# Optimization experiments

Hardware: AMD Instinct MI355X
Metric: run time of the kernel (lower is better)

The kernel has to match this reference:

```python
import jax, jax.numpy as jnp
import numpy as np

D_MODEL = 1024
N_HEADS = 16
D_HEAD = D_MODEL // N_HEADS
D_FF = 4096
BATCH = 2
SEQ = 2048
LN_EPS = 1e-5


def setup_inputs() -> dict:
    key = jax.random.key(0)
    ks = jax.random.split(key, 12)
    s = 1.0 / np.sqrt(D_MODEL)
    x = jax.random.normal(ks[0], (BATCH, SEQ, D_MODEL), dtype=jnp.float32)
    mask = jnp.broadcast_to(jnp.tril(jnp.ones((SEQ, SEQ), jnp.int32)), (BATCH, SEQ, SEQ))
    return {
        "x": x,
        "mask": mask,
        # per-head projections stacked: [H, D, Dh] (bias=False in source)
        "Wq": jax.random.normal(ks[1], (N_HEADS, D_MODEL, D_HEAD), jnp.float32) * s,
        "Wk": jax.random.normal(ks[2], (N_HEADS, D_MODEL, D_HEAD), jnp.float32) * s,
        "Wv": jax.random.normal(ks[3], (N_HEADS, D_MODEL, D_HEAD), jnp.float32) * s,
        "Wo": jax.random.normal(ks[4], (D_MODEL, D_MODEL), jnp.float32) * s,
        "ln1_w": jnp.ones((D_MODEL,), jnp.float32),
        "ln1_b": jnp.zeros((D_MODEL,), jnp.float32),
        "ln2_w": jnp.ones((D_MODEL,), jnp.float32),
        "ln2_b": jnp.zeros((D_MODEL,), jnp.float32),
        "W1": jax.random.normal(ks[5], (D_MODEL, D_FF), jnp.float32) * s,
        "b1": jnp.zeros((D_FF,), jnp.float32),
        "W2": jax.random.normal(ks[6], (D_FF, D_MODEL), jnp.float32) * (1.0 / np.sqrt(D_FF)),
        "b2": jnp.zeros((D_MODEL,), jnp.float32),
    }


def layer_norm(x, w, b):
    mu = jnp.mean(x, axis=-1, keepdims=True)
    var = jnp.var(x, axis=-1, keepdims=True)
    return (x - mu) * jax.lax.rsqrt(var + LN_EPS) * w + b


def reference(x, mask, Wq, Wk, Wv, Wo, ln1_w, ln1_b, ln2_w, ln2_b, W1, b1, W2, b2):
    # pre-LN masked self-attention
    h = layer_norm(x, ln1_w, ln1_b)
    q = jnp.einsum("bsd,hde->bhse", h, Wq)  # [B,H,S,Dh]
    k = jnp.einsum("bsd,hde->bhse", h, Wk)
    v = jnp.einsum("bsd,hde->bhse", h, Wv)
    scores = jnp.einsum("bhse,bhte->bhst", q, k) / np.sqrt(D_HEAD)
    scores = jnp.where(mask[:, None, :, :].astype(bool), scores, -jnp.inf)
    weights = jax.nn.softmax(scores, axis=-1)
    attn = jnp.einsum("bhst,bhte->bhse", weights, v)  # [B,H,S,Dh]
    # concat heads (head order = last-dim order in torch.cat)
    concat = attn.transpose(0, 2, 1, 3).reshape(x.shape[0], x.shape[1], D_MODEL)
    att_out = concat @ Wo
    att_x = x + att_out
    # FFN with exact (erf) GELU, matching nn.GELU default
    h2 = layer_norm(att_x, ln2_w, ln2_b)
    ff = jax.nn.gelu(h2 @ W1 + b1, approximate=False) @ W2 + b2
    return att_x + ff
```

## Files before the change

### kernel.cpp

```cpp
#include <hip/hip_runtime.h>
#include <hip/hip_bf16.h>
#include <math.h>

#define D_MODEL 1024
#define N_HEADS 16
#define D_HEAD  64
#define D_FF    4096
#define BATCH   2
#define SEQ     2048
#define NTOK    (BATCH*SEQ)

typedef __hip_bfloat16 bf16;
typedef __attribute__((ext_vector_type(8))) short short8;
typedef __attribute__((ext_vector_type(4))) float floatx4;

template<typename TIN>
__global__ void ln_kernel(const TIN* __restrict__ x,
                          const float* __restrict__ w,
                          const float* __restrict__ b,
                          bf16* __restrict__ out) {
    int row = blockIdx.x;
    int tid = threadIdx.x;
    const long base = (long)row * D_MODEL;
    float v[4];
    float s = 0.f, sq = 0.f;
#pragma unroll
    for (int i = 0; i < 4; ++i) {
        float xv = (float)x[base + tid + i*256];
        v[i] = xv; s += xv; sq += xv*xv;
    }
    __shared__ float r1[256], r2[256];
    r1[tid] = s; r2[tid] = sq; __syncthreads();
    for (int off = 128; off > 0; off >>= 1) {
        if (tid < off) { r1[tid] += r1[tid+off]; r2[tid] += r2[tid+off]; }
        __syncthreads();
    }
    float mean = r1[0] * (1.f/D_MODEL);
    float var  = r2[0] * (1.f/D_MODEL) - mean*mean;
    float rstd = rsqrtf(var + 1e-5f);
#pragma unroll
    for (int i = 0; i < 4; ++i) {
        int c = tid + i*256;
        out[base + c] = __float2bfloat16((v[i] - mean) * rstd * w[c] + b[c]);
    }
}

__global__ __launch_bounds__(256) void wcvt_kernel(const float* __restrict__ W,
                                                   bf16* __restrict__ Wt,
                                                   int K, int N) {
    __shared__ float t[32][33];
    int n0 = blockIdx.x * 32, k0 = blockIdx.y * 32;
    int lx = threadIdx.x & 31, ly = threadIdx.x >> 5;
#pragma unroll
    for (int i = 0; i < 4; ++i) {
        int k = ly + i * 8;
        t[k][lx] = W[(long)(k0 + k) * N + n0 + lx];
    }
    __syncthreads();
#pragma unroll
    for (int i = 0; i < 4; ++i) {
        int n = ly + i * 8;
        Wt[(long)(n0 + n) * K + k0 + lx] = __float2bfloat16(t[lx][n]);
    }
}

__global__ __launch_bounds__(256) void wcvt_wo_w1(const float* __restrict__ Wo,
                                                  const float* __restrict__ W1,
                                                  bf16* __restrict__ wo_bf,
                                                  bf16* __restrict__ w1_bf) {
    __shared__ float t[32][33];
    int gx = blockIdx.x;
    const float* W; bf16* Wt; int N, n0;
    if (gx < 32) { W = Wo; Wt = wo_bf; N = D_MODEL; n0 = gx * 32; }
    else         { W = W1; Wt = w1_bf; N = D_FF;    n0 = (gx - 32) * 32; }
    int k0 = blockIdx.y * 32;
    int lx = threadIdx.x & 31, ly = threadIdx.x >> 5;
#pragma unroll
    for (int i = 0; i < 4; ++i) {
        int k = ly + i * 8;
        t[k][lx] = W[(long)(k0 + k) * N + n0 + lx];
    }
    __syncthreads();
#pragma unroll
    for (int i = 0; i < 4; ++i) {
        int n = ly + i * 8;
        Wt[(long)(n0 + n) * D_MODEL + k0 + lx] = __float2bfloat16(t[lx][n]);
    }
}

__global__ __launch_bounds__(256) void wcvt_qkv(const float* __restrict__ Wq,
                                                const float* __restrict__ Wk,
                                                const float* __restrict__ Wv,
                                                bf16* __restrict__ outp) {
    __shared__ float t[32][33];
    int z = blockIdx.z, mat = z >> 4, head = z & 15;
    const float* W = (mat == 0 ? Wq : mat == 1 ? Wk : Wv) + (long)head * D_MODEL * D_HEAD;
    bf16* Wt = outp + (long)z * D_HEAD * D_MODEL;
    int n0 = blockIdx.x * 32, k0 = blockIdx.y * 32;
    int lx = threadIdx.x & 31, ly = threadIdx.x >> 5;
#pragma unroll
    for (int i = 0; i < 4; ++i) {
        int k = ly + i * 8;
        t[k][lx] = W[(long)(k0 + k) * D_HEAD + n0 + lx];
    }
    __syncthreads();
#pragma unroll
    for (int i = 0; i < 4; ++i) {
        int n = ly + i * 8;
        Wt[(long)(n0 + n) * D_MODEL + k0 + lx] = __float2bfloat16(t[lx][n]);
    }
}

__device__ inline void swz2d(int& bx, int& by) {
    int gx = gridDim.x;
    int nwg = gx * gridDim.y;
    int bid = blockIdx.y * gx + blockIdx.x;
    int swz = (bid & 7) * (nwg >> 3) + (bid >> 3);
    bx = swz % gx;
    by = swz / gx;
}

template<int ROWS>
__device__ inline void stage_tile(const bf16* g, int gstride, short* lds) {
    int lane = threadIdx.x & 63, wave = threadIdx.x >> 6;
#pragma unroll
    for (int it = 0; it < ROWS / 64; ++it) {
        int c = wave + it * 4;
        const bf16* gp = g + (long)(c * 16 + (lane >> 2)) * gstride + (lane & 3) * 8;
        short* lp = lds + c * 512 + lane * 8;
        __builtin_amdgcn_global_load_lds(
            (const __attribute__((address_space(1))) void*)gp,
            (__attribute__((address_space(3))) void*)lp, 16, 0, 0);
    }
}

template<int BM, int BN, int BK>
__device__ inline void gemm_accum(const bf16* __restrict__ A, int lda,
                                  const bf16* __restrict__ Wt, int K,
                                  int row0, int col0, short* As, short* Bs,
                                  floatx4 (&acc)[BM/32][BN/32]) {
    constexpr int MI  = BM / 32;
    constexpr int NR  = BN / 32;
    constexpr int ASZ = BM * BK;
    constexpr int BSZ = BN * BK;
    int tid  = threadIdx.x;
    int wave = tid >> 6, lane = tid & 63;
    int quad = lane >> 4, l16 = lane & 15;
    int wm = (wave >> 1) * (BM / 2);
    int wn = (wave & 1) * (BN / 2);

    auto stage = [&](int k0, int buf) {
#pragma unroll
        for (int kk = 0; kk < BK; kk += 32) {
            stage_tile<BM>(A  + (long)row0 * lda + k0 + kk, lda,
                           As + buf * ASZ + (kk / 32) * BM * 32);
            stage_tile<BN>(Wt + (long)col0 * K   + k0 + kk, K,
                           Bs + buf * BSZ + (kk / 32) * BN * 32);
        }
    };

    stage(0, 0);
    __syncthreads();

    int cur = 0;
    for (int k0 = 0; k0 < K; k0 += BK) {
        if (k0 + BK < K) stage(k0 + BK, cur ^ 1);

#pragma unroll
        for (int p = 0; p < BK / 32; ++p) {
            const short* Ap = As + cur * ASZ + p * BM * 32;
            const short* Bp = Bs + cur * BSZ + p * BN * 32;
            short8 af[MI], bfr[NR];
#pragma unroll
            for (int mi = 0; mi < MI; ++mi)
                af[mi] = *(const short8*)&Ap[(wm + mi * 16 + l16) * 32 + quad * 8];
#pragma unroll
            for (int ni = 0; ni < NR; ++ni)
                bfr[ni] = *(const short8*)&Bp[(wn + ni * 16 + l16) * 32 + quad * 8];
#pragma unroll
            for (int mi = 0; mi < MI; ++mi)
#pragma unroll
                for (int ni = 0; ni < NR; ++ni)
                    acc[mi][ni] = __builtin_amdgcn_mfma_f32_16x16x32_bf16(
                        af[mi], bfr[ni], acc[mi][ni], 0, 0, 0);
        }
        __syncthreads();
        cur ^= 1;
    }
}

template<int BM, int BN, int BK, int BIAS, int ACT, int RES, int OUTBF16>
__global__ __launch_bounds__(256) void mfma_gemm_bf(
    const bf16* __restrict__ A, int lda,
    const bf16* __restrict__ Wt, int K,
    const float* __restrict__ bias, const float* __restrict__ resid,
    void* __restrict__ Cout, int ldc)
{
    constexpr int MI = BM / 32;
    constexpr int NR = BN / 32;
    __shared__ short As[2 * BM * BK];
    __shared__ short Bs[2 * BN * BK];
    int bx, by; swz2d(bx, by);
    int row0 = by * BM, col0 = bx * BN;
    int tid = threadIdx.x, wave = tid >> 6, lane = tid & 63;
    int quad = lane >> 4, l16 = lane & 15;
    int wm = (wave >> 1) * (BM / 2);
    int wn = (wave & 1) * (BN / 2);

    floatx4 acc[MI][NR];
#pragma unroll
    for (int mi = 0; mi < MI; ++mi)
#pragma unroll
        for (int ni = 0; ni < NR; ++ni)
            acc[mi][ni] = (floatx4){0.f, 0.f, 0.f, 0.f};

    gemm_accum<BM, BN, BK>(A, lda, Wt, K, row0, col0, As, Bs, acc);

#pragma unroll
    for (int mi = 0; mi < MI; ++mi) {
#pragma unroll
        for (int ni = 0; ni < NR; ++ni) {
#pragma unroll
            for (int r = 0; r < 4; ++r) {
                int row = row0 + wm + mi * 16 + quad * 4 + r;
                int col = col0 + wn + ni * 16 + l16;
                float v = acc[mi][ni][r];
                if (BIAS) v += bias[col];
                if (ACT == 1) {
                    float x2 = v * v;
                    float arg = fminf(v * fmaf(0.1029392f, x2, 2.3021182f), 20.f);
                    float t = exp2f(arg);
                    v = v * t * __builtin_amdgcn_rcpf(t + 1.f);
                }
                long idx = (long)row * ldc + col;
                if (RES == 1) v += resid[idx];
                if (OUTBF16) ((bf16*)Cout)[idx] = __float2bfloat16(v);
                else         ((float*)Cout)[idx] = v;
            }
        }
    }
}


struct QkvOut { bf16* o[3]; };

#define RG(buf,mat,kh) (((buf)*4 + (mat)*2 + (kh)) * 8192)
#define G256_BAR  asm volatile("s_barrier" ::: "memory")
#define G256_VM4  asm volatile("s_waitcnt vmcnt(4)" ::: "memory")
#define G256_VM0  asm volatile("s_waitcnt vmcnt(0)" ::: "memory")

__device__ inline void stage2(const bf16* g0, const bf16* g1, int koff, short* lp) {
    __builtin_amdgcn_global_load_lds(
        (const __attribute__((address_space(1))) void*)(g0 + koff),
        (__attribute__((address_space(3))) void*)lp, 16, 0, 0);
    __builtin_amdgcn_global_load_lds(
        (const __attribute__((address_space(1))) void*)(g1 + koff),
        (__attribute__((address_space(3))) void*)(lp + 4096), 16, 0, 0);
}

template<int MH>
__device__ inline void rd_frags(const short* lds, int ra, int rb,
                                int wr, int wc, int l16, int quad,
                                short8 (&areg)[4], short8 (&breg)[4]) {
    if (MH == 0) {
#pragma unroll
        for (int ni = 0; ni < 4; ++ni) {
            int row = wc * 64 + ni * 16 + l16;
            int sl = quad ^ ((row >> 1) & 3);
            breg[ni] = *(const short8*)&lds[rb + row * 32 + sl * 8];
        }
    }
#pragma unroll
    for (int mi = 0; mi < 4; ++mi) {
        int row = wr * 128 + (MH * 4 + mi) * 16 + l16;
        int sl = quad ^ ((row >> 1) & 3);
        areg[mi] = *(const short8*)&lds[ra + row * 32 + sl * 8];
    }
}

template<int MH>
__device__ inline void do_mfma16(const short8 (&areg)[4], const short8 (&breg)[4],
                                 floatx4 (&acc)[8][4]) {
    __builtin_amdgcn_s_setprio(1);
#pragma unroll
    for (int mi = 0; mi < 4; ++mi)
#pragma unroll
        for (int ni = 0; ni < 4; ++ni)
            acc[MH * 4 + mi][ni] = __builtin_amdgcn_mfma_f32_16x16x32_bf16(
                areg[mi], breg[ni], acc[MH * 4 + mi][ni], 0, 0, 0);
    __builtin_amdgcn_s_setprio(0);
}

template<int EPI>
__global__ __launch_bounds__(512, 1) void gemm256_kernel(
    const bf16* __restrict__ A, int lda,
    const bf16* __restrict__ Wt, int K,
    const float* __restrict__ bias,
    bf16* __restrict__ Cout, int ldc, QkvOut qa)
{
    __shared__ short lds[65536];
    const int NT = K / 64;
    int row0 = blockIdx.y * 256, col0 = blockIdx.x * 256;
    int tid = threadIdx.x;
    int lane = tid & 63, wave = tid >> 6;
    int quad = lane >> 4, l16 = lane & 15;
    int wr = wave >> 2, wc = wave & 3;

    int srow = tid >> 2, slot = tid & 3;
    int cA0 = slot ^ ((srow >> 1) & 3);
    int cA1 = slot ^ (((srow + 128) >> 1) & 3);
    const bf16* a0 = A  + (long)(row0 + srow) * lda + cA0 * 8;
    const bf16* a1 = A  + (long)(row0 + srow + 128) * lda + cA1 * 8;
    const bf16* b0 = Wt + (long)(col0 + srow) * K + cA0 * 8;
    const bf16* b1 = Wt + (long)(col0 + srow + 128) * K + cA1 * 8;
    short* lt = lds + tid * 8;

    floatx4 acc[8][4];
#pragma unroll
    for (int mi = 0; mi < 8; ++mi)
#pragma unroll
        for (int ni = 0; ni < 4; ++ni)
            acc[mi][ni] = (floatx4){0.f, 0.f, 0.f, 0.f};

    stage2(a0, a1, 0,  lt + RG(0,0,0));
    stage2(b0, b1, 0,  lt + RG(0,1,0));
    stage2(a0, a1, 32, lt + RG(0,0,1));
    stage2(b0, b1, 32, lt + RG(0,1,1));
    stage2(a0, a1, 64, lt + RG(1,0,0));
    stage2(b0, b1, 64, lt + RG(1,1,0));
    G256_VM4;
    G256_BAR;

    short8 areg[4], breg[4];

    for (int i = 0; i < NT / 2; ++i) {
        int T = 2 * i;
        bool s2 = (T + 2 < NT);
        bool s3 = (T + 3 < NT);
        int k1off = (T + 1) * 64;
        int k2off = (T + 2) * 64;
        int k3off = (T + 3) * 64;

        rd_frags<0>(lds, RG(0,0,0), RG(0,1,0), wr, wc, l16, quad, areg, breg);
        stage2(a0, a1, k1off + 32, lt + RG(1,0,1));
        G256_BAR;
        do_mfma16<0>(areg, breg, acc);
        G256_BAR;

        rd_frags<1>(lds, RG(0,0,0), RG(0,1,0), wr, wc, l16, quad, areg, breg);
        stage2(b0, b1, k1off + 32, lt + RG(1,1,1));
        G256_BAR;
        do_mfma16<1>(areg, breg, acc);
        G256_BAR;

        rd_frags<0>(lds, RG(0,0,1), RG(0,1,1), wr, wc, l16, quad, areg, breg);
        if (s2) stage2(a0, a1, k2off, lt + RG(0,0,0));
        G256_BAR;
        do_mfma16<0>(areg, breg, acc);
        G256_BAR;

        rd_frags<1>(lds, RG(0,0,1), RG(0,1,1), wr, wc, l16, quad, areg, breg);
        if (s2) stage2(b0, b1, k2off, lt + RG(0,1,0));
        G256_BAR;
        do_mfma16<1>(areg, breg, acc);
        if (s2) { G256_VM4; } else { G256_VM0; }
        G256_BAR;

        rd_frags<0>(lds, RG(1,0,0), RG(1,1,0), wr, wc, l16, quad, areg, breg);
        if (s2) stage2(a0, a1, k2off + 32, lt + RG(0,0,1));
        G256_BAR;
        do_mfma16<0>(areg, breg, acc);
        G256_BAR;

        rd_frags<1>(lds, RG(1,0,0), RG(1,1,0), wr, wc, l16, quad, areg, breg);
        if (s2) stage2(b0, b1, k2off + 32, lt + RG(0,1,1));
        G256_BAR;
        do_mfma16<1>(areg, breg, acc);
        G256_BAR;

        rd_frags<0>(lds, RG(1,0,1), RG(1,1,1), wr, wc, l16, quad, areg, breg);
        if (s3) stage2(a0, a1, k3off, lt + RG(1,0,0));
        G256_BAR;
        do_mfma16<0>(areg, breg, acc);
        G256_BAR;

        rd_frags<1>(lds, RG(1,0,1), RG(1,1,1), wr, wc, l16, quad, areg, breg);
        if (s3) stage2(b0, b1, k3off, lt + RG(1,1,0));
        G256_BAR;
        do_mfma16<1>(areg, breg, acc);
        if (s3) { G256_VM4; } else { G256_VM0; }
        G256_BAR;
    }

#pragma unroll
    for (int mi = 0; mi < 8; ++mi) {
#pragma unroll
        for (int ni = 0; ni < 4; ++ni) {
#pragma unroll
            for (int r = 0; r < 4; ++r) {
                int row = row0 + wr * 128 + mi * 16 + quad * 4 + r;
                int col = col0 + wc * 64 + ni * 16 + l16;
                float v = acc[mi][ni][r];
                if constexpr (EPI == 0) {
                    v += bias[col];
                    float x2 = v * v;
                    float arg = fminf(v * fmaf(0.1029392f, x2, 2.3021182f), 20.f);
                    float t = exp2f(arg);
                    v = v * t * __builtin_amdgcn_rcpf(t + 1.f);
                    Cout[(long)row * ldc + col] = __float2bfloat16(v);
                } else {
                    int mat = col >> 10, hd = (col >> 6) & 15, d = col & 63;
                    int b = row >> 11, s = row & 2047;
                    qa.o[mat][(((long)(b * 16 + hd) * SEQ + s) << 6) + d] =
                        __float2bfloat16(v);
                }
            }
        }
    }
}

__global__ __launch_bounds__(256) void fattn_mfma(const bf16* __restrict__ q,
                                                  const bf16* __restrict__ k,
                                                  const bf16* __restrict__ v,
                                                  bf16* __restrict__ po,
                                                  float* __restrict__ lz) {
    int byr = blockIdx.y;
    int tile = (byr < 8) ? byr : 23 - byr;
    int chunk = blockIdx.z;
    int bh = blockIdx.x;
    int tid = threadIdx.x;
    int wave = tid >> 6, lane = tid & 63;
    int quad = lane >> 4, l16 = lane & 15;
    const long base = (long)bh * SEQ * D_HEAD;
    const int r0g = tile * 128;

    bf16*  pob = po + (long)chunk * 32 * SEQ * 64;
    float* lzb = lz + (long)chunk * 32 * SEQ;

    __shared__ short Ks[64 * 72];
    __shared__ short Vt[64 * 72];
    __shared__ short Ps[4][32 * 72];

    short8 qf[2][2];
#pragma unroll
    for (int rb = 0; rb < 2; ++rb) {
        const short* qrow = (const short*)(q + base +
            (long)(r0g + wave * 32 + rb * 16 + l16) * D_HEAD);
        qf[rb][0] = *(const short8*)(qrow + quad * 8);
        qf[rb][1] = *(const short8*)(qrow + 32 + quad * 8);
#pragma unroll
        for (int c = 0; c < 2; ++c)
#pragma unroll
            for (int j = 0; j < 8; ++j) {
                float f = __uint_as_float(((unsigned)(unsigned short)qf[rb][c][j]) << 16)
                          * 0.18033688f;
                qf[rb][c][j] = __builtin_bit_cast(short, __float2bfloat16(f));
            }
    }

    short8 onesf;
    {
        short o1 = (l16 == 0) ? (short)0x3F80 : (short)0;
#pragma unroll
        for (int j = 0; j < 8; ++j) onesf[j] = o1;
    }

    floatx4 o[2][4];
#pragma unroll
    for (int rb = 0; rb < 2; ++rb)
#pragma unroll
        for (int nb = 0; nb < 4; ++nb) o[rb][nb] = (floatx4){0.f, 0.f, 0.f, 0.f};
    floatx4 l4[2] = {(floatx4){0.f,0.f,0.f,0.f}, (floatx4){0.f,0.f,0.f,0.f}};

    const int kt0 = chunk ? tile + 1 : 0;
    const int kt1 = chunk ? 2 * tile + 1 : tile;
    for (int kt = kt0; kt <= kt1; ++kt) {
        __syncthreads();
        {
            int t = tid >> 2, c = tid & 3;
            const short* krow = (const short*)(k + base + (long)(kt * 64 + t) * D_HEAD);
            *(uint4*)&Ks[t * 72 + c * 16]     = *(const uint4*)(krow + c * 16);
            *(uint4*)&Ks[t * 72 + c * 16 + 8] = *(const uint4*)(krow + c * 16 + 8);
        }
        {
            int tp = (tid & 31) * 2;
            int d0 = ((tid >> 5) & 7) * 8;
            const short* v0 = (const short*)(v + base + (long)(kt * 64 + tp) * D_HEAD + d0);
            short va[8], vb[8];
            *(uint4*)va = *(const uint4*)v0;
            *(uint4*)vb = *(const uint4*)(v0 + D_HEAD);
#pragma unroll
            for (int j = 0; j < 8; ++j) {
                unsigned pk = (unsigned)(unsigned short)va[j] |
                              ((unsigned)(unsigned short)vb[j] << 16);
                *(unsigned*)&Vt[(d0 + j) * 72 + tp] = pk;
            }
        }
        __syncthreads();

        if (kt * 64 > r0g + wave * 32 + 31) continue;

        floatx4 s[2][4];
#pragma unroll
        for (int nb = 0; nb < 4; ++nb) {
            short8 kf0 = *(const short8*)&Ks[(nb * 16 + l16) * 72 + quad * 8];
            short8 kf1 = *(const short8*)&Ks[(nb * 16 + l16) * 72 + 32 + quad * 8];
#pragma unroll
            for (int rb = 0; rb < 2; ++rb) {
                floatx4 z4 = (floatx4){0.f, 0.f, 0.f, 0.f};
                z4 = __builtin_amdgcn_mfma_f32_16x16x32_bf16(qf[rb][0], kf0, z4, 0, 0, 0);
                z4 = __builtin_amdgcn_mfma_f32_16x16x32_bf16(qf[rb][1], kf1, z4, 0, 0, 0);
                s[rb][nb] = z4;
            }
        }

        if (kt >= 2 * tile) {
#pragma unroll
            for (int rb = 0; rb < 2; ++rb) {
                int qg = r0g + wave * 32 + rb * 16 + quad * 4;
#pragma unroll
                for (int nb = 0; nb < 4; ++nb) {
                    int kg = kt * 64 + nb * 16 + l16;
#pragma unroll
                    for (int r = 0; r < 4; ++r)
                        if (kg > qg + r) s[rb][nb][r] = -1e30f;
                }
            }
        }

        short* Pw = &Ps[wave][0];
#pragma unroll
        for (int rb = 0; rb < 2; ++rb)
#pragma unroll
            for (int nb = 0; nb < 4; ++nb)
#pragma unroll
                for (int r = 0; r < 4; ++r) {
                    float p = exp2f(s[rb][nb][r]);
                    Pw[(rb * 16 + quad * 4 + r) * 72 + nb * 16 + l16] =
                        __builtin_bit_cast(short, __float2bfloat16(p));
                }

        short8 pf[2][2];
#pragma unroll
        for (int rb = 0; rb < 2; ++rb) {
            pf[rb][0] = *(const short8*)&Pw[(rb * 16 + l16) * 72 + quad * 8];
            pf[rb][1] = *(const short8*)&Pw[(rb * 16 + l16) * 72 + 32 + quad * 8];
        }
#pragma unroll
        for (int nb = 0; nb < 4; ++nb) {
            short8 vf0 = *(const short8*)&Vt[(nb * 16 + l16) * 72 + quad * 8];
            short8 vf1 = *(const short8*)&Vt[(nb * 16 + l16) * 72 + 32 + quad * 8];
#pragma unroll
            for (int rb = 0; rb < 2; ++rb) {
                o[rb][nb] = __builtin_amdgcn_mfma_f32_16x16x32_bf16(pf[rb][0], vf0, o[rb][nb], 0, 0, 0);
                o[rb][nb] = __builtin_amdgcn_mfma_f32_16x16x32_bf16(pf[rb][1], vf1, o[rb][nb], 0, 0, 0);
            }
        }
#pragma unroll
        for (int rb = 0; rb < 2; ++rb) {
            l4[rb] = __builtin_amdgcn_mfma_f32_16x16x32_bf16(pf[rb][0], onesf, l4[rb], 0, 0, 0);
            l4[rb] = __builtin_amdgcn_mfma_f32_16x16x32_bf16(pf[rb][1], onesf, l4[rb], 0, 0, 0);
        }
    }

#pragma unroll
    for (int rb = 0; rb < 2; ++rb) {
#pragma unroll
        for (int nb = 0; nb < 4; ++nb)
#pragma unroll
            for (int r = 0; r < 4; ++r) {
                int row = r0g + wave * 32 + rb * 16 + quad * 4 + r;
                pob[((long)bh * SEQ + row) * 64 + nb * 16 + l16] =
                    __float2bfloat16(o[rb][nb][r]);
            }
        if (l16 == 0) {
#pragma unroll
            for (int r = 0; r < 4; ++r) {
                int row = r0g + wave * 32 + rb * 16 + quad * 4 + r;
                lzb[(long)bh * SEQ + row] = l4[rb][r];
            }
        }
    }
}

__global__ __launch_bounds__(256) void attn_combine(const bf16* __restrict__ po,
                                                    const float* __restrict__ lz,
                                                    bf16* __restrict__ cc) {
    const long CH = 32L * SEQ * 64;
    int row = blockIdx.x;
    int b = row >> 11, s = row & 2047;
    int tid = threadIdx.x;
    int col = tid * 4;
    int h = col >> 6, d = col & 63;
    long pidx = ((long)(b * 16 + h) * SEQ + s) * 64 + d;
    uint2 u0 = *(const uint2*)((const unsigned short*)po + pidx);
    uint2 u1 = *(const uint2*)((const unsigned short*)po + CH + pidx);
    long li = (long)(b * 16 + h) * SEQ + s;
    float linv = 1.f / (lz[li] + lz[32L * SEQ + li]);
    unsigned ua[4] = {u0.x & 0xFFFFu, u0.x >> 16, u0.y & 0xFFFFu, u0.y >> 16};
    unsigned ub[4] = {u1.x & 0xFFFFu, u1.x >> 16, u1.y & 0xFFFFu, u1.y >> 16};
    unsigned short rr[4];
#pragma unroll
    for (int i = 0; i < 4; ++i) {
        float ov = __uint_as_float(ua[i] << 16) + __uint_as_float(ub[i] << 16);
        rr[i] = __builtin_bit_cast(unsigned short, __float2bfloat16(ov * linv));
    }
    uint2 w;
    w.x = (unsigned)rr[0] | ((unsigned)rr[1] << 16);
    w.y = (unsigned)rr[2] | ((unsigned)rr[3] << 16);
    *(uint2*)((unsigned short*)cc + (long)row * D_MODEL + col) = w;
}

extern "C" void kernel_launch(void* const* d_in, const int* in_sizes, int n_in,
                              void* d_out, int out_size, void* d_ws, size_t ws_size,
                              hipStream_t stream) {
    const float* x    = (const float*)d_in[0];
    const float* Wq   = (const float*)d_in[2];
    const float* Wk   = (const float*)d_in[3];
    const float* Wv   = (const float*)d_in[4];
    const float* Wo   = (const float*)d_in[5];
    const float* ln1w = (const float*)d_in[6];
    const float* ln1b = (const float*)d_in[7];
    const float* ln2w = (const float*)d_in[8];
    const float* ln2b = (const float*)d_in[9];
    const float* W1   = (const float*)d_in[10];
    const float* b1   = (const float*)d_in[11];
    const float* W2   = (const float*)d_in[12];
    const float* b2   = (const float*)d_in[13];
    float* out = (float*)d_out;

    char* wsb = (char*)d_ws;
    const size_t MB = 1024*1024;
    bf16*  h1      = (bf16*)(wsb + 0*MB);
    bf16*  qb      = (bf16*)(wsb + 8*MB);
    bf16*  kb      = (bf16*)(wsb + 16*MB);
    bf16*  vb      = (bf16*)(wsb + 24*MB);
    bf16*  wqkv_bf = (bf16*)(wsb + 32*MB);
    bf16*  po      = (bf16*)(wsb + 32*MB);
    float* lz      = (float*)(wsb + 48*MB);
    bf16*  cc      = (bf16*)(wsb + 0*MB);
    bf16*  wo_bf   = (bf16*)(wsb + 8*MB);
    bf16*  w1_bf   = (bf16*)(wsb + 10*MB);
    bf16*  h2      = (bf16*)(wsb + 0*MB);
    bf16*  ff      = (bf16*)(wsb + 24*MB);
    bf16*  w2_bf   = (bf16*)(wsb + 8*MB);

    QkvOut qa; qa.o[0] = qb; qa.o[1] = kb; qa.o[2] = vb;
    QkvOut qdummy = {};

    ln_kernel<float><<<NTOK, 256, 0, stream>>>(x, ln1w, ln1b, h1);

    wcvt_qkv<<<dim3(2, 32, 48), 256, 0, stream>>>(Wq, Wk, Wv, wqkv_bf);

    gemm256_kernel<1><<<dim3(12, 16), 512, 0, stream>>>(
        h1, D_MODEL, wqkv_bf, D_MODEL, nullptr, nullptr, 0, qa);

    fattn_mfma<<<dim3(BATCH*N_HEADS, SEQ/128, 2), 256, 0, stream>>>(qb, kb, vb, po, lz);

    attn_combine<<<NTOK, 256, 0, stream>>>(po, lz, cc);

    wcvt_wo_w1<<<dim3(160, 32), 256, 0, stream>>>(Wo, W1, wo_bf, w1_bf);

    mfma_gemm_bf<64,128,64,0,0,1,0><<<dim3(8,64), 256, 0, stream>>>(
        cc, D_MODEL, wo_bf, D_MODEL, nullptr, x, out, D_MODEL);

    ln_kernel<float><<<NTOK, 256, 0, stream>>>(out, ln2w, ln2b, h2);

    gemm256_kernel<0><<<dim3(16, 16), 512, 0, stream>>>(
        h2, D_MODEL, w1_bf, D_MODEL, b1, ff, D_FF, qdummy);

    wcvt_kernel<<<dim3(D_MODEL/32, D_FF/32), 256, 0, stream>>>(W2, w2_bf, D_FF, D_MODEL);

    mfma_gemm_bf<64,128,64,1,0,1,0><<<dim3(8,64), 256, 0, stream>>>(
        ff, D_FF, w2_bf, D_FF, b2, out, out, D_MODEL);
}
```

Before: 382.4 us.

## Route Wo and W2 projections through 256x256 GEMM with split-K atomics for W2

Replaces the generic 64x128 tiled GEMM used for the output projection and second FFN matmul with the 256x256 tile gemm256 kernel, which gains two new epilogues. The Wo projection adds the residual in its epilogue. The W2 projection splits K=4096 into 4 slices along grid z and accumulates into the existing fp32 output with atomicAdd, adding bias only in slice 0. The aim is better data reuse and MFMA efficiency, at the cost of a small grid for Wo (64 blocks) and atomic traffic plus order-dependent float summation for W2.

```diff
diff --git a/kernel.cpp b/kernel.cpp
--- a/kernel.cpp
+++ b/kernel.cpp
@@ -111,136 +111,6 @@
     }
 }
 
-__device__ inline void swz2d(int& bx, int& by) {
-    int gx = gridDim.x;
-    int nwg = gx * gridDim.y;
-    int bid = blockIdx.y * gx + blockIdx.x;
-    int swz = (bid & 7) * (nwg >> 3) + (bid >> 3);
-    bx = swz % gx;
-    by = swz / gx;
-}
-
-template<int ROWS>
-__device__ inline void stage_tile(const bf16* g, int gstride, short* lds) {
-    int lane = threadIdx.x & 63, wave = threadIdx.x >> 6;
-#pragma unroll
-    for (int it = 0; it < ROWS / 64; ++it) {
-        int c = wave + it * 4;
-        const bf16* gp = g + (long)(c * 16 + (lane >> 2)) * gstride + (lane & 3) * 8;
-        short* lp = lds + c * 512 + lane * 8;
-        __builtin_amdgcn_global_load_lds(
-            (const __attribute__((address_space(1))) void*)gp,
-            (__attribute__((address_space(3))) void*)lp, 16, 0, 0);
-    }
-}
-
-template<int BM, int BN, int BK>
-__device__ inline void gemm_accum(const bf16* __restrict__ A, int lda,
-                                  const bf16* __restrict__ Wt, int K,
-                                  int row0, int col0, short* As, short* Bs,
-                                  floatx4 (&acc)[BM/32][BN/32]) {
-    constexpr int MI  = BM / 32;
-    constexpr int NR  = BN / 32;
-    constexpr int ASZ = BM * BK;
-    constexpr int BSZ = BN * BK;
-    int tid  = threadIdx.x;
-    int wave = tid >> 6, lane = tid & 63;
-    int quad = lane >> 4, l16 = lane & 15;
-    int wm = (wave >> 1) * (BM / 2);
-    int wn = (wave & 1) * (BN / 2);
-
-    auto stage = [&](int k0, int buf) {
-#pragma unroll
-        for (int kk = 0; kk < BK; kk += 32) {
-            stage_tile<BM>(A  + (long)row0 * lda + k0 + kk, lda,
-                           As + buf * ASZ + (kk / 32) * BM * 32);
-            stage_tile<BN>(Wt + (long)col0 * K   + k0 + kk, K,
-                           Bs + buf * BSZ + (kk / 32) * BN * 32);
-        }
-    };
-
-    stage(0, 0);
-    __syncthreads();
-
-    int cur = 0;
-    for (int k0 = 0; k0 < K; k0 += BK) {
-        if (k0 + BK < K) stage(k0 + BK, cur ^ 1);
-
-#pragma unroll
-        for (int p = 0; p < BK / 32; ++p) {
-            const short* Ap = As + cur * ASZ + p * BM * 32;
-            const short* Bp = Bs + cur * BSZ + p * BN * 32;
-            short8 af[MI], bfr[NR];
-#pragma unroll
-            for (int mi = 0; mi < MI; ++mi)
-                af[mi] = *(const short8*)&Ap[(wm + mi * 16 + l16) * 32 + quad * 8];
-#pragma unroll
-            for (int ni = 0; ni < NR; ++ni)
-                bfr[ni] = *(const short8*)&Bp[(wn + ni * 16 + l16) * 32 + quad * 8];
-#pragma unroll
-            for (int mi = 0; mi < MI; ++mi)
-#pragma unroll
-                for (int ni = 0; ni < NR; ++ni)
-                    acc[mi][ni] = __builtin_amdgcn_mfma_f32_16x16x32_bf16(
-                        af[mi], bfr[ni], acc[mi][ni], 0, 0, 0);
-        }
-        __syncthreads();
-        cur ^= 1;
-    }
-}
-
-template<int BM, int BN, int BK, int BIAS, int ACT, int RES, int OUTBF16>
-__global__ __launch_bounds__(256) void mfma_gemm_bf(
-    const bf16* __restrict__ A, int lda,
-    const bf16* __restrict__ Wt, int K,
-    const float* __restrict__ bias, const float* __restrict__ resid,
-    void* __restrict__ Cout, int ldc)
-{
-    constexpr int MI = BM / 32;
-    constexpr int NR = BN / 32;
-    __shared__ short As[2 * BM * BK];
-    __shared__ short Bs[2 * BN * BK];
-    int bx, by; swz2d(bx, by);
-    int row0 = by * BM, col0 = bx * BN;
-    int tid = threadIdx.x, wave = tid >> 6, lane = tid & 63;
-    int quad = lane >> 4, l16 = lane & 15;
-    int wm = (wave >> 1) * (BM / 2);
-    int wn = (wave & 1) * (BN / 2);
-
-    floatx4 acc[MI][NR];
-#pragma unroll
-    for (int mi = 0; mi < MI; ++mi)
-#pragma unroll
-        for (int ni = 0; ni < NR; ++ni)
-            acc[mi][ni] = (floatx4){0.f, 0.f, 0.f, 0.f};
-
-    gemm_accum<BM, BN, BK>(A, lda, Wt, K, row0, col0, As, Bs, acc);
-
-#pragma unroll
-    for (int mi = 0; mi < MI; ++mi) {
-#pragma unroll
-        for (int ni = 0; ni < NR; ++ni) {
-#pragma unroll
-            for (int r = 0; r < 4; ++r) {
-                int row = row0 + wm + mi * 16 + quad * 4 + r;
-                int col = col0 + wn + ni * 16 + l16;
-                float v = acc[mi][ni][r];
-                if (BIAS) v += bias[col];
-                if (ACT == 1) {
-                    float x2 = v * v;
-                    float arg = fminf(v * fmaf(0.1029392f, x2, 2.3021182f), 20.f);
-                    float t = exp2f(arg);
-                    v = v * t * __builtin_amdgcn_rcpf(t + 1.f);
-                }
-                long idx = (long)row * ldc + col;
-                if (RES == 1) v += resid[idx];
-                if (OUTBF16) ((bf16*)Cout)[idx] = __float2bfloat16(v);
-                else         ((float*)Cout)[idx] = v;
-            }
-        }
-    }
-}
-
 
 struct QkvOut { bf16* o[3]; };
 
@@ -294,13 +164,14 @@
 template<int EPI>
 __global__ __launch_bounds__(512, 1) void gemm256_kernel(
     const bf16* __restrict__ A, int lda,
-    const bf16* __restrict__ Wt, int K,
-    const float* __restrict__ bias,
-    bf16* __restrict__ Cout, int ldc, QkvOut qa)
+    const bf16* __restrict__ Wt, int ldw, int K,
+    const float* __restrict__ bias, const float* __restrict__ resid,
+    bf16* __restrict__ Cout, float* __restrict__ fout, int ldc, QkvOut qa)
 {
     __shared__ short lds[65536];
     const int NT = K / 64;
     int row0 = blockIdx.y * 256, col0 = blockIdx.x * 256;
+    long zoff = (long)blockIdx.z * K;
     int tid = threadIdx.x;
     int lane = tid & 63, wave = tid >> 6;
     int quad = lane >> 4, l16 = lane & 15;
@@ -309,10 +180,10 @@
     int srow = tid >> 2, slot = tid & 3;
     int cA0 = slot ^ ((srow >> 1) & 3);
     int cA1 = slot ^ (((srow + 128) >> 1) & 3);
-    const bf16* a0 = A  + (long)(row0 + srow) * lda + cA0 * 8;
-    const bf16* a1 = A  + (long)(row0 + srow + 128) * lda + cA1 * 8;
-    const bf16* b0 = Wt + (long)(col0 + srow) * K + cA0 * 8;
-    const bf16* b1 = Wt + (long)(col0 + srow + 128) * K + cA1 * 8;
+    const bf16* a0 = A  + zoff + (long)(row0 + srow) * lda + cA0 * 8;
+    const bf16* a1 = A  + zoff + (long)(row0 + srow + 128) * lda + cA1 * 8;
+    const bf16* b0 = Wt + zoff + (long)(col0 + srow) * ldw + cA0 * 8;
+    const bf16* b1 = Wt + zoff + (long)(col0 + srow + 128) * ldw + cA1 * 8;
     short* lt = lds + tid * 8;
 
     floatx4 acc[8][4];
@@ -408,11 +279,17 @@
                     float t = exp2f(arg);
                     v = v * t * __builtin_amdgcn_rcpf(t + 1.f);
                     Cout[(long)row * ldc + col] = __float2bfloat16(v);
-                } else {
+                } else if constexpr (EPI == 1) {
                     int mat = col >> 10, hd = (col >> 6) & 15, d = col & 63;
                     int b = row >> 11, s = row & 2047;
                     qa.o[mat][(((long)(b * 16 + hd) * SEQ + s) << 6) + d] =
                         __float2bfloat16(v);
+                } else if constexpr (EPI == 2) {
+                    if (blockIdx.z == 0) v += bias[col];
+                    atomicAdd(&fout[(long)row * ldc + col], v);
+                } else {
+                    long idx = (long)row * ldc + col;
+                    fout[idx] = v + resid[idx];
                 }
             }
         }
@@ -653,7 +530,8 @@
     wcvt_qkv<<<dim3(2, 32, 48), 256, 0, stream>>>(Wq, Wk, Wv, wqkv_bf);
 
     gemm256_kernel<1><<<dim3(12, 16), 512, 0, stream>>>(
-        h1, D_MODEL, wqkv_bf, D_MODEL, nullptr, nullptr, 0, qa);
+        h1, D_MODEL, wqkv_bf, D_MODEL, D_MODEL, nullptr, nullptr,
+        nullptr, nullptr, 0, qa);
 
     fattn_mfma<<<dim3(BATCH*N_HEADS, SEQ/128, 2), 256, 0, stream>>>(qb, kb, vb, po, lz);
 
@@ -661,16 +539,19 @@
 
     wcvt_wo_w1<<<dim3(160, 32), 256, 0, stream>>>(Wo, W1, wo_bf, w1_bf);
 
-    mfma_gemm_bf<64,128,64,0,0,1,0><<<dim3(8,64), 256, 0, stream>>>(
-        cc, D_MODEL, wo_bf, D_MODEL, nullptr, x, out, D_MODEL);
+    gemm256_kernel<3><<<dim3(4, 16), 512, 0, stream>>>(
+        cc, D_MODEL, wo_bf, D_MODEL, D_MODEL, nullptr, x,
+        nullptr, out, D_MODEL, qdummy);
 
     ln_kernel<float><<<NTOK, 256, 0, stream>>>(out, ln2w, ln2b, h2);
 
     gemm256_kernel<0><<<dim3(16, 16), 512, 0, stream>>>(
-        h2, D_MODEL, w1_bf, D_MODEL, b1, ff, D_FF, qdummy);
+        h2, D_MODEL, w1_bf, D_MODEL, D_MODEL, b1, nullptr,
+        ff, nullptr, D_FF, qdummy);
 
     wcvt_kernel<<<dim3(D_MODEL/32, D_FF/32), 256, 0, stream>>>(W2, w2_bf, D_FF, D_MODEL);
 
-    mfma_gemm_bf<64,128,64,1,0,1,0><<<dim3(8,64), 256, 0, stream>>>(
-        ff, D_FF, w2_bf, D_FF, b2, out, out, D_MODEL);
-}
+    gemm256_kernel<2><<<dim3(4, 16, 4), 512, 0, stream>>>(
+        ff, D_FF, w2_bf, D_FF, D_MODEL, b2, nullptr,
+        nullptr, out, D_MODEL, qdummy);
+}
```

After: 445.8 us. 16.6% more time.
